# Kernel tuning notes

Measured on AMD Instinct MI355X. Metric: run time of the kernel, lower is better.

## Reference

```python
import jax, jax.numpy as jnp
import numpy as np

B, M, D = 8192, 64, 256
NEG = -1e9  # masking value for invalid (padded) memory slots


def setup_inputs() -> dict:
    key = jax.random.key(0)
    ks = jax.random.split(key, 8)
    s = 1.0 / np.sqrt(D)  # nn.Linear default init scale
    return {
        "h_tilde": jax.random.normal(ks[0], (B, D), jnp.float32),
        "mem": jax.random.normal(ks[1], (B, M, D), jnp.float32),
        "lengths": jax.random.randint(ks[2], (B,), 0, M + 1, jnp.int32),
        "Wg_w": jax.random.uniform(ks[3], (D, D), jnp.float32, -s, s),
        "Wg_b": jax.random.uniform(ks[4], (D,), jnp.float32, -s, s),
        "Ug_w": jax.random.uniform(ks[5], (D, D), jnp.float32, -s, s),
        "Ug_b": jax.random.uniform(ks[6], (D,), jnp.float32, -s, s),
        "b_g": jnp.zeros((D,), jnp.float32),
    }


def reference(h_tilde, mem, lengths, Wg_w, Wg_b, Ug_w, Ug_b, b_g):
    # valid-slot mask: [B, M]
    valid = jnp.arange(M)[None, :] < lengths[:, None]
    # per-sample attention over ragged memory
    scores = jnp.einsum("bmd,bd->bm", mem, h_tilde)          # [B, M]
    attn = jax.nn.softmax(jnp.where(valid, scores, NEG), axis=1)
    r = jnp.einsum("bm,bmd->bd", attn, mem)                   # [B, D]
    # gated fusion (two Linears + extra bias)
    g = jax.nn.sigmoid(h_tilde @ Wg_w.T + Wg_b + r @ Ug_w.T + Ug_b + b_g)
    fused = g * r + (1.0 - g) * h_tilde
    # empty-memory samples pass through h_tilde unchanged
    has_mem = (lengths > 0)[:, None]
    return jnp.where(has_mem, fused, h_tilde)
```

## Files before the change

### kernel.cpp

```cpp
#include <hip/hip_runtime.h>
#include <hip/hip_bf16.h>

#define BB 8192
#define MM 64
#define DD 256
#define NEGV -1e9f
#define TSTR 260

typedef __attribute__((ext_vector_type(8))) short frag_ab;
typedef __attribute__((ext_vector_type(4))) float f32x4;

struct __align__(8) bfq { __hip_bfloat162 lo, hi; };

__device__ inline short f2bs(float f) {
    __hip_bfloat16 v = __float2bfloat16(f);
    return *reinterpret_cast<short*>(&v);
}

__global__ __launch_bounds__(256) void attn_kernel(
    const float* __restrict__ h, const float* __restrict__ mem,
    const int* __restrict__ len, float* __restrict__ r_out)
{
    __shared__ __hip_bfloat16 tile[MM * TSTR];
    __shared__ __align__(16) float h_s[DD];
    __shared__ float score_s[MM];
    __shared__ __align__(16) float attn_s[MM];

    const int b = blockIdx.x;
    const int t = threadIdx.x;
    const int m = t >> 2;
    const int c = t & 3;
    const int L = len[b];

    h_s[t] = h[(size_t)b * DD + t];
    __syncthreads();

    const float* mrow = mem + (size_t)b * MM * DD + (size_t)m * DD + c * 64;
    __hip_bfloat16* trow = tile + m * TSTR + c * 64;

    float p = 0.f;
    #pragma unroll
    for (int j = 0; j < 16; ++j) {
        const float4 v  = *reinterpret_cast<const float4*>(mrow + 4 * j);
        const float4 hv = *reinterpret_cast<const float4*>(h_s + c * 64 + 4 * j);
        p += v.x * hv.x + v.y * hv.y + v.z * hv.z + v.w * hv.w;
        bfq q;
        q.lo = __float22bfloat162_rn(float2{v.x, v.y});
        q.hi = __float22bfloat162_rn(float2{v.z, v.w});
        *reinterpret_cast<bfq*>(trow + 4 * j) = q;
    }
    p += __shfl_xor(p, 1, 64);
    p += __shfl_xor(p, 2, 64);
    if (c == 0) score_s[m] = (m < L) ? p : NEGV;
    __syncthreads();

    if (t < 64) {
        const float s = score_s[t];
        float mx = s;
        #pragma unroll
        for (int off = 32; off > 0; off >>= 1)
            mx = fmaxf(mx, __shfl_xor(mx, off, 64));
        const float e = __expf(s - mx);
        float den = e;
        #pragma unroll
        for (int off = 32; off > 0; off >>= 1)
            den += __shfl_xor(den, off, 64);
        attn_s[t] = e / den;
    }
    __syncthreads();

    float acc = 0.f;
    #pragma unroll
    for (int mc = 0; mc < 16; ++mc) {
        const float4 aw = *reinterpret_cast<const float4*>(attn_s + 4 * mc);
        acc += aw.x * __bfloat162float(tile[(4 * mc + 0) * TSTR + t]);
        acc += aw.y * __bfloat162float(tile[(4 * mc + 1) * TSTR + t]);
        acc += aw.z * __bfloat162float(tile[(4 * mc + 2) * TSTR + t]);
        acc += aw.w * __bfloat162float(tile[(4 * mc + 3) * TSTR + t]);
    }
    r_out[(size_t)b * DD + t] = acc;
}

__global__ __launch_bounds__(256) void gate_kernel(
    const float* __restrict__ h, const float* __restrict__ r,
    const int* __restrict__ len,
    const float* __restrict__ Wg_w, const float* __restrict__ Wg_b,
    const float* __restrict__ Ug_w, const float* __restrict__ Ug_b,
    const float* __restrict__ b_g, float* __restrict__ out)
{
    __shared__ __hip_bfloat16 Abuf[64 * 32];
    __shared__ __hip_bfloat16 Wbuf[64 * 32];

    const int t    = threadIdx.x;
    const int lane = t & 63;
    const int wave = t >> 6;
    const int brow0 = blockIdx.x * 64;
    const int dcol0 = blockIdx.y * 64;

    const int srow = t >> 2;
    const int skq  = t & 3;

    const f32x4 zero = {0.f, 0.f, 0.f, 0.f};
    f32x4 acc[4];
    #pragma unroll
    for (int ct = 0; ct < 4; ++ct) acc[ct] = zero;

    const int arow_m = (lane & 15);
    const int kchunk = (lane >> 4) * 8;

    for (int phase = 0; phase < 2; ++phase) {
        const float* Ag = phase ? r : h;
        const float* Wg = phase ? Ug_w : Wg_w;
        const float* ap = Ag + (size_t)(brow0 + srow) * DD + skq * 8;
        const float* wp = Wg + (size_t)(dcol0 + srow) * DD + skq * 8;

        for (int k0 = 0; k0 < DD; k0 += 32) {
            const float4 a0 = *reinterpret_cast<const float4*>(ap + k0);
            const float4 a1 = *reinterpret_cast<const float4*>(ap + k0 + 4);
            const float4 w0 = *reinterpret_cast<const float4*>(wp + k0);
            const float4 w1 = *reinterpret_cast<const float4*>(wp + k0 + 4);

            __syncthreads();
            frag_ab av, wv;
            av[0] = f2bs(a0.x); av[1] = f2bs(a0.y); av[2] = f2bs(a0.z); av[3] = f2bs(a0.w);
            av[4] = f2bs(a1.x); av[5] = f2bs(a1.y); av[6] = f2bs(a1.z); av[7] = f2bs(a1.w);
            wv[0] = f2bs(w0.x); wv[1] = f2bs(w0.y); wv[2] = f2bs(w0.z); wv[3] = f2bs(w0.w);
            wv[4] = f2bs(w1.x); wv[5] = f2bs(w1.y); wv[6] = f2bs(w1.z); wv[7] = f2bs(w1.w);
            *reinterpret_cast<frag_ab*>(&Abuf[srow * 32 + skq * 8]) = av;
            *reinterpret_cast<frag_ab*>(&Wbuf[srow * 32 + skq * 8]) = wv;
            __syncthreads();

            const frag_ab af = *reinterpret_cast<const frag_ab*>(
                &Abuf[(wave * 16 + arow_m) * 32 + kchunk]);
            #pragma unroll
            for (int ct = 0; ct < 4; ++ct) {
                const frag_ab wf = *reinterpret_cast<const frag_ab*>(
                    &Wbuf[(ct * 16 + arow_m) * 32 + kchunk]);
                acc[ct] = __builtin_amdgcn_mfma_f32_16x16x32_bf16(af, wf, acc[ct], 0, 0, 0);
            }
        }
    }

    float bias_v[4];
    #pragma unroll
    for (int ct = 0; ct < 4; ++ct) {
        const int d = dcol0 + ct * 16 + (lane & 15);
        bias_v[ct] = Wg_b[d] + Ug_b[d] + b_g[d];
    }
    const int rbase = brow0 + wave * 16 + (lane >> 4) * 4;
    #pragma unroll
    for (int i = 0; i < 4; ++i) {
        const int bb = rbase + i;
        const int lb = len[bb];
        #pragma unroll
        for (int ct = 0; ct < 4; ++ct) {
            const int d = dcol0 + ct * 16 + (lane & 15);
            const float x = acc[ct][i] + bias_v[ct];
            const float g = 1.f / (1.f + __expf(-x));
            const size_t idx = (size_t)bb * DD + d;
            const float rv = r[idx];
            const float hv = h[idx];
            out[idx] = (lb > 0) ? (hv + g * (rv - hv)) : hv;
        }
    }
}

extern "C" void kernel_launch(void* const* d_in, const int* in_sizes, int n_in,
                              void* d_out, int out_size, void* d_ws, size_t ws_size,
                              hipStream_t stream) {
    const float* h    = (const float*)d_in[0];
    const float* mem  = (const float*)d_in[1];
    const int*   len  = (const int*)d_in[2];
    const float* Wg_w = (const float*)d_in[3];
    const float* Wg_b = (const float*)d_in[4];
    const float* Ug_w = (const float*)d_in[5];
    const float* Ug_b = (const float*)d_in[6];
    const float* b_g  = (const float*)d_in[7];
    float* out  = (float*)d_out;
    float* r_ws = (float*)d_ws;

    attn_kernel<<<BB, 256, 0, stream>>>(h, mem, len, r_ws);
    gate_kernel<<<dim3(BB / 64, DD / 64), 256, 0, stream>>>(
        h, r_ws, len, Wg_w, Wg_b, Ug_w, Ug_b, b_g, out);
}
```

Measured before the change: 715.6 us.

## Keep memory tile in registers and reorganize attention reduction across waves

The attention kernel now has each wave load 16 memory rows with lanes spanning the feature dimension, keeping the bf16-converted tile in registers instead of shared memory. Score partials are written to a padded shared array and reduced per row, and the weighted sum is computed per wave in registers, then combined across the four waves through shared memory. This removes the large shared bf16 tile and its strided reads, and launch bounds request higher occupancy. In exchange it adds register pressure, an extra barrier and a cross-wave partial-sum step.

Result: no change. 720.3 us (+0.7%).

```diff
diff --git a/kernel.cpp b/kernel.cpp
--- a/kernel.cpp
+++ b/kernel.cpp
@@ -5,53 +5,62 @@
 #define MM 64
 #define DD 256
 #define NEGV -1e9f
-#define TSTR 260
+#define PSTR 68
 
 typedef __attribute__((ext_vector_type(8))) short frag_ab;
 typedef __attribute__((ext_vector_type(4))) float f32x4;
-
-struct __align__(8) bfq { __hip_bfloat162 lo, hi; };
 
 __device__ inline short f2bs(float f) {
     __hip_bfloat16 v = __float2bfloat16(f);
     return *reinterpret_cast<short*>(&v);
 }
-
-__global__ __launch_bounds__(256) void attn_kernel(
+__device__ inline float blo(unsigned w) { return __uint_as_float(w << 16); }
+__device__ inline float bhi(unsigned w) { return __uint_as_float(w & 0xffff0000u); }
+
+__global__ __launch_bounds__(256, 6) void attn_kernel(
     const float* __restrict__ h, const float* __restrict__ mem,
     const int* __restrict__ len, float* __restrict__ r_out)
 {
-    __shared__ __hip_bfloat16 tile[MM * TSTR];
-    __shared__ __align__(16) float h_s[DD];
+    __shared__ float part[MM * PSTR];
     __shared__ float score_s[MM];
     __shared__ __align__(16) float attn_s[MM];
-
-    const int b = blockIdx.x;
-    const int t = threadIdx.x;
-    const int m = t >> 2;
-    const int c = t & 3;
-    const int L = len[b];
-
-    h_s[t] = h[(size_t)b * DD + t];
-    __syncthreads();
-
-    const float* mrow = mem + (size_t)b * MM * DD + (size_t)m * DD + c * 64;
-    __hip_bfloat16* trow = tile + m * TSTR + c * 64;
-
-    float p = 0.f;
-    #pragma unroll
-    for (int j = 0; j < 16; ++j) {
-        const float4 v  = *reinterpret_cast<const float4*>(mrow + 4 * j);
-        const float4 hv = *reinterpret_cast<const float4*>(h_s + c * 64 + 4 * j);
-        p += v.x * hv.x + v.y * hv.y + v.z * hv.z + v.w * hv.w;
-        bfq q;
-        q.lo = __float22bfloat162_rn(float2{v.x, v.y});
-        q.hi = __float22bfloat162_rn(float2{v.z, v.w});
-        *reinterpret_cast<bfq*>(trow + 4 * j) = q;
-    }
-    p += __shfl_xor(p, 1, 64);
-    p += __shfl_xor(p, 2, 64);
-    if (c == 0) score_s[m] = (m < L) ? p : NEGV;
+    __shared__ __align__(16) float rpart[4 * DD];
+
+    const int b    = blockIdx.x;
+    const int t    = threadIdx.x;
+    const int lane = t & 63;
+    const int wave = t >> 6;
+    const int L    = len[b];
+
+    const float4 hv = *reinterpret_cast<const float4*>(h + (size_t)b * DD + 4 * lane);
+    const float* mbase = mem + (size_t)b * MM * DD + (size_t)(wave * 16) * DD + 4 * lane;
+
+    unsigned tile[32];
+    float p[16];
+    #pragma unroll
+    for (int i = 0; i < 16; ++i) {
+        const float4 v = *reinterpret_cast<const float4*>(mbase + i * DD);
+        p[i] = v.x * hv.x + v.y * hv.y + v.z * hv.z + v.w * hv.w;
+        __hip_bfloat162 q0 = __float22bfloat162_rn(float2{v.x, v.y});
+        __hip_bfloat162 q1 = __float22bfloat162_rn(float2{v.z, v.w});
+        tile[2 * i]     = *reinterpret_cast<unsigned*>(&q0);
+        tile[2 * i + 1] = *reinterpret_cast<unsigned*>(&q1);
+    }
+    #pragma unroll
+    for (int i = 0; i < 16; ++i)
+        part[(wave * 16 + i) * PSTR + lane] = p[i];
+    __syncthreads();
+
+    {
+        const int m = t >> 2, c = t & 3;
+        const float4* pr = reinterpret_cast<const float4*>(part + m * PSTR + c * 16);
+        const float4 s0 = pr[0], s1 = pr[1], s2 = pr[2], s3 = pr[3];
+        float s = (s0.x + s0.y + s0.z + s0.w) + (s1.x + s1.y + s1.z + s1.w)
+                + (s2.x + s2.y + s2.z + s2.w) + (s3.x + s3.y + s3.z + s3.w);
+        s += __shfl_xor(s, 1, 64);
+        s += __shfl_xor(s, 2, 64);
+        if (c == 0) score_s[m] = (m < L) ? s : NEGV;
+    }
     __syncthreads();
 
     if (t < 64) {
@@ -69,16 +78,25 @@
     }
     __syncthreads();
 
-    float acc = 0.f;
-    #pragma unroll
-    for (int mc = 0; mc < 16; ++mc) {
-        const float4 aw = *reinterpret_cast<const float4*>(attn_s + 4 * mc);
-        acc += aw.x * __bfloat162float(tile[(4 * mc + 0) * TSTR + t]);
-        acc += aw.y * __bfloat162float(tile[(4 * mc + 1) * TSTR + t]);
-        acc += aw.z * __bfloat162float(tile[(4 * mc + 2) * TSTR + t]);
-        acc += aw.w * __bfloat162float(tile[(4 * mc + 3) * TSTR + t]);
-    }
-    r_out[(size_t)b * DD + t] = acc;
+    float4 rp = {0.f, 0.f, 0.f, 0.f};
+    #pragma unroll
+    for (int ic = 0; ic < 4; ++ic) {
+        const float4 aw = *reinterpret_cast<const float4*>(attn_s + wave * 16 + 4 * ic);
+        const float a[4] = {aw.x, aw.y, aw.z, aw.w};
+        #pragma unroll
+        for (int k = 0; k < 4; ++k) {
+            const int i = 4 * ic + k;
+            rp.x += a[k] * blo(tile[2 * i]);
+            rp.y += a[k] * bhi(tile[2 * i]);
+            rp.z += a[k] * blo(tile[2 * i + 1]);
+            rp.w += a[k] * bhi(tile[2 * i + 1]);
+        }
+    }
+    *reinterpret_cast<float4*>(rpart + wave * DD + 4 * lane) = rp;
+    __syncthreads();
+
+    const float r = rpart[t] + rpart[DD + t] + rpart[2 * DD + t] + rpart[3 * DD + t];
+    r_out[(size_t)b * DD + t] = r;
 }
 
 __global__ __launch_bounds__(256) void gate_kernel(
@@ -159,8 +177,8 @@
             const float g = 1.f / (1.f + __expf(-x));
             const size_t idx = (size_t)bb * DD + d;
             const float rv = r[idx];
-            const float hv = h[idx];
-            out[idx] = (lb > 0) ? (hv + g * (rv - hv)) : hv;
+            const float hvv = h[idx];
+            out[idx] = (lb > 0) ? (hvv + g * (rv - hvv)) : hvv;
         }
     }
 }
```
